# Kernel tuning notes

Hardware: AMD Instinct MI355X
Metric: run time of the kernel (lower is better)

Reference implementation:

```python
import jax, jax.numpy as jnp
import numpy as np

B, T, D_OBS = 64, 512, 128
D_LAT, D_HID, K = 16, 256, 8
VAR = 0.0005
LOG2PI = float(np.log(2.0 * np.pi))


def _leaky(x):
    return jnp.where(x > 0, x, 0.01 * x)


def setup_inputs() -> dict:
    key = jax.random.key(0)
    ks = jax.random.split(key, 12)
    s = 0.05
    return {
        "x": jax.random.normal(ks[0], (B, T, D_OBS), jnp.float32),
        "eps": jax.random.normal(ks[1], (B, T, D_LAT), jnp.float32),
        "W1": jax.random.normal(ks[2], (D_OBS, D_HID), jnp.float32) * s,
        "b1": jnp.zeros((D_HID,), jnp.float32),
        "W2": jax.random.normal(ks[3], (D_HID, 2 * D_LAT), jnp.float32) * s,
        "b2": jnp.zeros((2 * D_LAT,), jnp.float32),
        "Wt1": jax.random.normal(ks[4], (K, D_LAT, D_HID), jnp.float32) * s,
        "bt1": jnp.zeros((K, D_HID), jnp.float32),
        "Wt2": jax.random.normal(ks[5], (K, D_HID, D_LAT), jnp.float32) * s,
        "bt2": jnp.zeros((K, D_LAT), jnp.float32),
        "Wd1": jax.random.normal(ks[6], (D_LAT, D_HID), jnp.float32) * s,
        "bd1": jnp.zeros((D_HID,), jnp.float32),
        "Wd2": jax.random.normal(ks[7], (D_HID, D_OBS), jnp.float32) * s,
        "bd2": jnp.zeros((D_OBS,), jnp.float32),
        "Q": jax.random.normal(ks[8], (K, K), jnp.float32) * 0.1,
        "pi": jax.random.normal(ks[9], (K,), jnp.float32) * 0.1,
        "init_mean": jax.random.normal(ks[10], (K, D_LAT), jnp.float32),
        "init_cov": jax.random.uniform(ks[11], (K, 1, 1), jnp.float32) * jnp.eye(D_LAT, dtype=jnp.float32)[None] * 5.0,
        "covs": jnp.tile(jnp.eye(D_LAT, dtype=jnp.float32)[None], (K, 1, 1)),
    }


def _mvn_logprob(diff, chol):
    # diff [..., K, d]; chol [K, d, d] lower Cholesky of per-state covariance
    d = chol.shape[-1]
    Linv = jax.scipy.linalg.solve_triangular(
        chol, jnp.broadcast_to(jnp.eye(d, dtype=chol.dtype), chol.shape), lower=True)
    sol = jnp.einsum('kij,...kj->...ki', Linv, diff)
    logdet = 2.0 * jnp.sum(jnp.log(jnp.diagonal(chol, axis1=-2, axis2=-1)), -1)  # [K]
    return -0.5 * (d * LOG2PI + logdet + jnp.sum(sol * sol, -1))


def _forward(x, eps, W1, b1, W2, b2, Wt1, bt1, Wt2, bt2, Wd1, bd1, Wd2, bd2,
             Q, pi, init_mean, init_cov, covs):
    Bx = x.shape[0]
    dz = init_mean.shape[-1]
    # ---- factored MLP encoder: x -> (mu, logvar); reparameterized sample ----
    h = _leaky(x @ W1 + b1)
    enc = h @ W2 + b2
    z_mu, z_log_var = enc[..., :dz], enc[..., dz:]
    z = z_mu + jnp.exp(0.5 * z_log_var) * eps                            # [B,T,dz]
    # ---- local evidence log p(z_t | z_{t-1}, s_t=k) ----
    jitter = 1e-6 * jnp.eye(dz, dtype=x.dtype)
    L0 = jnp.linalg.cholesky(init_cov @ jnp.swapaxes(init_cov, -1, -2) + jitter)
    ev1 = _mvn_logprob(z[:, 0:1, None, :] - init_mean[None, None], L0)   # [B,1,K]
    ht = jax.nn.softplus(jnp.einsum('btd,kdh->btkh', z[:, :-1], Wt1) + bt1)
    means = jnp.einsum('btkh,khd->btkd', ht, Wt2) + bt2                  # [B,T-1,K,dz]
    Lt = jnp.linalg.cholesky(covs @ jnp.swapaxes(covs, -1, -2) + jitter)
    evT = _mvn_logprob(z[:, 1:, None, :] - means, Lt)                    # [B,T-1,K]
    ev = jnp.concatenate([ev1, evT], axis=1)                             # [B,T,K]
    # ---- HMM alpha recursion in log domain (temperature=1) ----
    log_pi = jax.nn.log_softmax(pi)
    Qlog = jax.nn.log_softmax(Q, axis=-1).T                              # [new, old]
    lp0 = ev[:, 0] + log_pi
    lZ0 = jax.scipy.special.logsumexp(lp0, axis=-1)
    la0 = lp0 - lZ0[:, None]

    def step(la, ev_t):
        lp = jax.scipy.special.logsumexp(ev_t[:, :, None] + Qlog[None] + la[:, None, :], axis=-1)
        lZ = jax.scipy.special.logsumexp(lp, axis=-1)
        return lp - lZ[:, None], lZ

    _, lZs = jax.lax.scan(step, la0, jnp.moveaxis(ev[:, 1:], 1, 0))
    log_Z = lZ0 + jnp.sum(lZs, axis=0)                                   # [B]
    # ---- decoder ----
    x_hat = _leaky(z @ Wd1 + bd1) @ Wd2 + bd2
    # ---- ELBO ----
    recon = jnp.sum(-0.5 * jnp.log(2.0 * jnp.pi * VAR) - (x - x_hat) ** 2 / (2.0 * VAR)) / Bx
    logq = -0.5 * (dz * LOG2PI + jnp.sum(z_log_var, -1)
                   + jnp.sum((z - z_mu) ** 2 / jnp.exp(z_log_var), -1))
    entropy_q = -jnp.sum(logq) / Bx
    msm = jnp.sum(log_Z) / Bx
    loss = -(recon + entropy_q + msm)
    return x_hat, z, loss


def reference(x, eps, W1, b1, W2, b2, Wt1, bt1, Wt2, bt2, Wd1, bd1, Wd2, bd2,
              Q, pi, init_mean, init_cov, covs):
    return _forward(x, eps, W1, b1, W2, b2, Wt1, bt1, Wt2, bt2, Wd1, bd1, Wd2, bd2,
                    Q, pi, init_mean, init_cov, covs)
```

## Files before the change

kernel.cpp:

```cpp
#include <hip/hip_runtime.h>
#include <math.h>

#define B_SZ   64
#define T_SZ   512
#define DOBS   128
#define DLAT   16
#define DHID   256
#define K_SZ   8
#define ROWS_A 32768

#define LOG2PI_F 1.8378770664093453f
#define VAR_F    5.0e-4f

#define LINV0_OFF   16
#define LOGDET0_OFF 2064
#define LINVT_OFF   2080
#define LOGDETT_OFF 4128
#define CVEC_OFF    4224
#define WIMG_F_OFF  8192

#define EVT_W1   0
#define EVT_W2   49152
#define EVT_LINV 82944
#define ENC_W1   86016
#define ENC_W2   120832
#define DEC_W1   129280
#define DEC_W2   135424
#define WCVT_TOTAL 182272

#define Z_OUT_OFF   4194304
#define LOSS_OFF    4718592
#define PBUF_OFF  262144

typedef __attribute__((ext_vector_type(8))) short short8;
typedef __attribute__((ext_vector_type(8))) unsigned short ush8;
typedef __attribute__((ext_vector_type(4))) float floatx4;

__device__ __forceinline__ float leakyf(float v) { return v > 0.f ? v : 0.01f * v; }
__device__ __forceinline__ unsigned short f2bf(float f) {
  union { float f; unsigned int u; } v; v.f = f;
  unsigned int lsb = (v.u >> 16) & 1;
  v.u += 0x7fffu + lsb;
  return (unsigned short)(v.u >> 16);
}
__device__ __forceinline__ unsigned int cvt_pk_bf16(float lo, float hi) {
  unsigned int r;
  asm("v_cvt_pk_bf16_f32 %0, %1, %2" : "=v"(r) : "v"(lo), "v"(hi));
  return r;
}
__device__ __forceinline__ float softplus_fast(float v) {
  return __logf(1.f + __expf(v));
}
__device__ __forceinline__ int permk(int kk) {
  return (kk & ~31) | ((kk & 15) << 1) | ((kk >> 4) & 1);
}

__global__ __launch_bounds__(256) void prep_kernel(const float* __restrict__ init_cov,
                                                   const float* __restrict__ covs,
                                                   const float* __restrict__ Wt2,
                                                   const float* __restrict__ bt2,
                                                   float* __restrict__ ws,
                                                   float* __restrict__ w2l) {
  __shared__ float M[16][16];
  __shared__ float L[16][16];
  __shared__ float X[16][17];
  int job = blockIdx.x;
  const float* C = (job < 8) ? (init_cov + job * 256) : (covs + (job - 8) * 256);
  float* linv = ws + ((job < 8) ? (LINV0_OFF + job * 256) : (LINVT_OFF + (job - 8) * 256));
  float* logdet = ws + ((job < 8) ? (LOGDET0_OFF + job) : (LOGDETT_OFF + (job - 8)));
  int tid = threadIdx.x;
  if (job == 0 && tid < 8) ws[tid] = 0.f;
  int i = tid >> 4, j = tid & 15;
  {
    float s = (i == j) ? 1e-6f : 0.f;
    #pragma unroll
    for (int p = 0; p < 16; ++p) s += C[i * 16 + p] * C[j * 16 + p];
    M[i][j] = s;
  }
  __syncthreads();
  for (int c = 0; c < 16; ++c) {
    if (tid == 0) {
      float s = M[c][c];
      for (int p = 0; p < c; ++p) s -= L[c][p] * L[c][p];
      L[c][c] = sqrtf(s);
    }
    __syncthreads();
    if (tid > c && tid < 16) {
      float s = M[tid][c];
      for (int p = 0; p < c; ++p) s -= L[tid][p] * L[c][p];
      L[tid][c] = s / L[c][c];
    }
    __syncthreads();
  }
  if (tid < 16) {
    for (int r = 0; r < 16; ++r) {
      float s = (r == tid) ? 1.f : 0.f;
      for (int p = tid; p < r; ++p) s -= L[r][p] * X[p][tid];
      X[r][tid] = (r >= tid) ? s / L[r][r] : 0.f;
    }
  }
  __syncthreads();
  linv[i * 16 + j] = X[i][j];
  if (tid == 0) {
    float s = 0.f;
    for (int d = 0; d < 16; ++d) s += logf(L[d][d]);
    *logdet = 2.f * s;
  }
  if (job >= 8) {
    int k = job - 8;
    const float* wrow = Wt2 + (long)k * 4096 + tid * 16;
    float* orow = w2l + (long)k * 4096 + tid * 16;
    #pragma unroll
    for (int i2 = 0; i2 < 16; ++i2) {
      float s = 0.f;
      for (int jj = 0; jj <= i2; ++jj) s += wrow[jj] * X[i2][jj];
      orow[i2] = s;
    }
    if (tid < 16) {
      float s = 0.f;
      const float* b = bt2 + k * 16;
      for (int jj = 0; jj <= tid; ++jj) s += b[jj] * X[tid][jj];
      ws[CVEC_OFF + k * 16 + tid] = s;
    }
  }
}

__global__ __launch_bounds__(256) void wcvt_kernel(
    const float* __restrict__ Wt1, const float* __restrict__ bt1,
    const float* __restrict__ W1, const float* __restrict__ W2,
    const float* __restrict__ Wd1, const float* __restrict__ bd1,
    const float* __restrict__ Wd2,
    const float* __restrict__ ws, const float* __restrict__ w2l,
    unsigned short* __restrict__ wimg) {
  for (int e = blockIdx.x * 256 + threadIdx.x; e < WCVT_TOTAL; e += gridDim.x * 256) {
    if (e < 65536) {
      int k = e >> 13, r = e & 8191, ch = r >> 5, d = r & 31;
      if (d < 24) {
        float v = (d < 16) ? Wt1[k * 4096 + d * 256 + ch]
                           : ((d == 16) ? bt1[k * 256 + ch] : 0.f);
        wimg[EVT_W1 + k * 6144 + ch * 24 + d] = f2bf(v);
      }
    } else if (e < 98304) {
      int e2 = e - 65536; int k = e2 >> 12, r = e2 & 4095, d2 = r >> 8, h = r & 255;
      wimg[EVT_W2 + k * 4224 + d2 * 264 + permk(h)] = f2bf(w2l[(long)k * 4096 + h * 16 + d2]);
    } else if (e < 100352) {
      int e2 = e - 98304; int k = e2 >> 8, r = e2 & 255, i = r >> 4, j = r & 15;
      wimg[EVT_LINV + k * 384 + i * 24 + j] = f2bf(ws[LINVT_OFF + k * 256 + i * 16 + j]);
    } else if (e < 133120) {
      int e2 = e - 100352; int n = e2 >> 7, kk = e2 & 127;
      wimg[ENC_W1 + n * 136 + kk] = f2bf(W1[kk * 256 + n]);
    } else if (e < 141312) {
      int e2 = e - 133120; int n = e2 >> 8, kk = e2 & 255;
      wimg[ENC_W2 + n * 264 + permk(kk)] = f2bf(W2[kk * 32 + n]);
    } else if (e < 149504) {
      int e2 = e - 141312; int n = e2 >> 5, d = e2 & 31;
      if (d < 24) {
        float v = (d < 16) ? Wd1[d * 256 + n] : ((d == 16) ? bd1[n] : 0.f);
        wimg[DEC_W1 + n * 24 + d] = f2bf(v);
      }
    } else {
      int e2 = e - 149504; int kk = e2 >> 7, n = e2 & 127;
      wimg[DEC_W2 + n * 264 + permk(kk)] = f2bf(Wd2[kk * 128 + n]);
    }
  }
}

__global__ __launch_bounds__(256) void enc_kernel(
    const float* __restrict__ x, const float* __restrict__ eps,
    const float* __restrict__ b1, const float* __restrict__ b2,
    const unsigned short* __restrict__ wimg,
    float* __restrict__ z_out, float* __restrict__ ws) {
  __shared__ __align__(16) unsigned short w2t[32 * 264];
  __shared__ __align__(16) unsigned short ttile[4][16 * 56];
  __shared__ float b1s[256];
  __shared__ float sred;
  int tid = threadIdx.x;
  if (tid == 0) sred = 0.f;
  {
    const ush8* s2 = (const ush8*)(wimg + ENC_W2);
    for (int e = tid; e < 1056; e += 256) ((ush8*)w2t)[e] = s2[e];
    b1s[tid] = b1[tid];
  }
  __syncthreads();

  int wid = tid >> 6, lane = tid & 63;
  int m = lane & 15, quad = lane >> 4;
  unsigned short* tt = ttile[wid];
  const unsigned short* w1i = wimg + ENC_W1;
  long rowb = (long)blockIdx.x * 64 + wid * 16;

  short8 xa[4];
  const float* xp = x + (rowb + m) * 128 + quad * 8;
  #pragma unroll
  for (int kt = 0; kt < 4; ++kt) {
    float4 f0 = *(const float4*)(xp + kt * 32);
    float4 f1 = *(const float4*)(xp + kt * 32 + 4);
    union { unsigned int u[4]; short8 s; } cv;
    cv.u[0] = cvt_pk_bf16(f0.x, f0.y);
    cv.u[1] = cvt_pk_bf16(f0.z, f0.w);
    cv.u[2] = cvt_pk_bf16(f1.x, f1.y);
    cv.u[3] = cvt_pk_bf16(f1.z, f1.w);
    xa[kt] = cv.s;
  }
  float bm0 = b2[m], bm1 = b2[16 + m];
  floatx4 a20 = {bm0, bm0, bm0, bm0};
  floatx4 a21 = {bm1, bm1, bm1, bm1};
  #pragma unroll
  for (int cp = 0; cp < 8; ++cp) {
    floatx4 a1h[2];
    #pragma unroll
    for (int h = 0; h < 2; ++h) {
      int c = cp * 2 + h;
      float bias = b1s[c * 16 + m];
      floatx4 a1 = {bias, bias, bias, bias};
      #pragma unroll
      for (int kt = 0; kt < 4; ++kt) {
        short8 bf = *(const short8*)&w1i[(c * 16 + m) * 136 + kt * 32 + quad * 8];
        a1 = __builtin_amdgcn_mfma_f32_16x16x32_bf16(xa[kt], bf, a1, 0, 0, 0);
      }
      a1h[h] = a1;
    }
    #pragma unroll
    for (int g = 0; g < 4; ++g) {
      unsigned int p = cvt_pk_bf16(leakyf(a1h[0][g]), leakyf(a1h[1][g]));
      *(unsigned int*)&tt[(quad * 4 + g) * 56 + 2 * m] = p;
    }
    short8 ha = *(const short8*)&tt[m * 56 + quad * 8];
    short8 wb0 = *(const short8*)&w2t[m * 264 + cp * 32 + quad * 8];
    short8 wb1 = *(const short8*)&w2t[(16 + m) * 264 + cp * 32 + quad * 8];
    a20 = __builtin_amdgcn_mfma_f32_16x16x32_bf16(ha, wb0, a20, 0, 0, 0);
    a21 = __builtin_amdgcn_mfma_f32_16x16x32_bf16(ha, wb1, a21, 0, 0, 0);
  }
  float logq_acc = 0.f;
  #pragma unroll
  for (int g = 0; g < 4; ++g) {
    long row = rowb + quad * 4 + g;
    float mu = a20[g], lv = a21[g];
    float ev = eps[row * 16 + m];
    float zv = mu + __expf(0.5f * lv) * ev;
    z_out[row * 16 + m] = zv;
    float zz = zv - mu;
    logq_acc += lv + zz * zz * __expf(-lv);
  }
  #pragma unroll
  for (int off = 1; off < 64; off <<= 1) logq_acc += __shfl_xor(logq_acc, off, 64);
  if (lane == 0) atomicAdd(&sred, -0.5f * logq_acc);
  __syncthreads();
  if (tid == 0) atomicAdd(&ws[1], sred - 0.5f * 16.f * LOG2PI_F * 64.f);
}

__global__ __launch_bounds__(256, 8) void evt_kernel(
    const float* __restrict__ z, const unsigned short* __restrict__ wimg,
    const float* __restrict__ ws, float* __restrict__ evT) {
  __shared__ __align__(16) unsigned short w2t[4224];
  __shared__ __align__(16) unsigned short ttile[4][16 * 56];
  __shared__ __align__(16) unsigned short linvb[384];
  int tid = threadIdx.x;
  int k = blockIdx.y;
  {
    const ush8* s2 = (const ush8*)(wimg + EVT_W2 + k * 4224);
    for (int e = tid; e < 528; e += 256) ((ush8*)w2t)[e] = s2[e];
    if (tid < 48) ((ush8*)linvb)[tid] = ((const ush8*)(wimg + EVT_LINV + k * 384))[tid];
  }
  float logdetk = ws[LOGDETT_OFF + k];
  __syncthreads();

  int wid = tid >> 6, lane = tid & 63;
  int m = lane & 15, quad = lane >> 4;
  unsigned short* tt = ttile[wid];
  const unsigned short* w1i = wimg + EVT_W1 + k * 6144;
  float cval = ws[CVEC_OFF + k * 16 + m];

  for (int tile = 0; tile < 2; ++tile) {
    long rowb = (long)blockIdx.x * 128 + wid * 32 + tile * 16;
    short8 za = (short8)0;
    if (quad < 2) {
      const float* zp = z + (rowb + m) * 16 + quad * 8;
      float4 f0 = *(const float4*)zp;
      float4 f1 = *(const float4*)(zp + 4);
      union { unsigned int u[4]; short8 s; } cv;
      cv.u[0] = cvt_pk_bf16(f0.x, f0.y);
      cv.u[1] = cvt_pk_bf16(f0.z, f0.w);
      cv.u[2] = cvt_pk_bf16(f1.x, f1.y);
      cv.u[3] = cvt_pk_bf16(f1.z, f1.w);
      za = cv.s;
    } else if (quad == 2) {
      za[0] = (short)0x3F80;
    }
    short8 za2 = (short8)0;
    if (quad < 2) {
      long r2 = rowb + m + 1; if (r2 > 32767) r2 = 32767;
      const float* zp2 = z + r2 * 16 + quad * 8;
      float4 f0 = *(const float4*)zp2;
      float4 f1 = *(const float4*)(zp2 + 4);
      union { unsigned int u[4]; short8 s; } cv;
      cv.u[0] = cvt_pk_bf16(f0.x, f0.y);
      cv.u[1] = cvt_pk_bf16(f0.z, f0.w);
      cv.u[2] = cvt_pk_bf16(f1.x, f1.y);
      cv.u[3] = cvt_pk_bf16(f1.z, f1.w);
      za2 = cv.s;
    }
    floatx4 a2 = {cval, cval, cval, cval};
    #pragma unroll
    for (int cp = 0; cp < 8; ++cp) {
      floatx4 a1h[2];
      #pragma unroll
      for (int h = 0; h < 2; ++h) {
        int c = cp * 2 + h;
        short8 bfrag = (short8)0;
        if (quad < 3) bfrag = *(const short8*)&w1i[(c * 16 + m) * 24 + quad * 8];
        floatx4 a1 = {0.f, 0.f, 0.f, 0.f};
        a1 = __builtin_amdgcn_mfma_f32_16x16x32_bf16(za, bfrag, a1, 0, 0, 0);
        a1h[h] = a1;
      }
      #pragma unroll
      for (int g = 0; g < 4; ++g) {
        unsigned int p = cvt_pk_bf16(softplus_fast(a1h[0][g]), softplus_fast(a1h[1][g]));
        *(unsigned int*)&tt[(quad * 4 + g) * 56 + 2 * m] = p;
      }
      short8 ha = *(const short8*)&tt[m * 56 + quad * 8];
      short8 wb = *(const short8*)&w2t[m * 264 + cp * 32 + quad * 8];
      a2 = __builtin_amdgcn_mfma_f32_16x16x32_bf16(ha, wb, a2, 0, 0, 0);
    }
    short8 lb = (short8)0;
    if (quad < 2) lb = *(const short8*)&linvb[m * 24 + quad * 8];
    floatx4 a3 = {0.f, 0.f, 0.f, 0.f};
    a3 = __builtin_amdgcn_mfma_f32_16x16x32_bf16(za2, lb, a3, 0, 0, 0);
    #pragma unroll
    for (int g = 0; g < 4; ++g) {
      float v = a3[g] - a2[g];
      v = v * v;
      v += __shfl_xor(v, 1, 64);
      v += __shfl_xor(v, 2, 64);
      v += __shfl_xor(v, 4, 64);
      v += __shfl_xor(v, 8, 64);
      long grow = rowb + quad * 4 + g;
      if (m == 0 && (grow & 511) != 511) {
        long r1 = grow + 1;
        evT[(r1 >> 9) * 4096 + (long)k * 512 + (r1 & 511)] =
            -0.5f * (16.f * LOG2PI_F + logdetk + v);
      }
    }
  }
}

__global__ __launch_bounds__(1024) void hmm_fused(
    const float* __restrict__ Q, const float* __restrict__ pi,
    const float* __restrict__ z, const float* __restrict__ init_mean,
    const float* __restrict__ evT, float* __restrict__ ws) {
  __shared__ float sP[16][64];
  __shared__ float sacc[16];
  int tid = threadIdx.x;
  int c = tid >> 6, lane = tid & 63;
  int b = blockIdx.x;
  int i = lane >> 3, j = lane & 7;

  float qp[8];
  #pragma unroll
  for (int p = 0; p < 8; ++p) {
    float mr = Q[p * 8 + 0];
    #pragma unroll
    for (int cc = 1; cc < 8; ++cc) mr = fmaxf(mr, Q[p * 8 + cc]);
    float rs = 0.f;
    #pragma unroll
    for (int cc = 0; cc < 8; ++cc) rs += __expf(Q[p * 8 + cc] - mr);
    qp[p] = __expf(Q[p * 8 + i] - mr) / rs;
  }
  float qself;
  {
    float mr = Q[j * 8 + 0];
    #pragma unroll
    for (int cc = 1; cc < 8; ++cc) mr = fmaxf(mr, Q[j * 8 + cc]);
    float rs = 0.f;
    #pragma unroll
    for (int cc = 0; cc < 8; ++cc) rs += __expf(Q[j * 8 + cc] - mr);
    qself = __expf(Q[j * 8 + i] - mr) / rs;
  }

  int t0 = 1 + c * 32;
  int L = (c == 15) ? 31 : 32;
  const float* evI = evT + (long)b * 4096 + (long)i * 512 + t0;

  float f[32];
  float accm = 0.f;
  #pragma unroll
  for (int s = 0; s < 32; ++s) {
    float e = (s < L) ? evI[s] : 0.f;
    float m = e;
    m = fmaxf(m, __shfl_xor(m, 8, 64));
    m = fmaxf(m, __shfl_xor(m, 16, 64));
    m = fmaxf(m, __shfl_xor(m, 32, 64));
    f[s] = __expf(e - m);
    if (s < L) accm += m;
  }

  float P = f[0] * qself;
  #pragma unroll
  for (int s = 1; s < 32; ++s) {
    if (s < L) {
      float a0 = __shfl(P, j,      64);
      float a1 = __shfl(P, 8 + j,  64);
      float a2 = __shfl(P, 16 + j, 64);
      float a3 = __shfl(P, 24 + j, 64);
      float a4 = __shfl(P, 32 + j, 64);
      float a5 = __shfl(P, 40 + j, 64);
      float a6 = __shfl(P, 48 + j, 64);
      float a7 = __shfl(P, 56 + j, 64);
      float sv = ((qp[0] * a0 + qp[1] * a1) + (qp[2] * a2 + qp[3] * a3))
               + ((qp[4] * a4 + qp[5] * a5) + (qp[6] * a6 + qp[7] * a7));
      P = f[s] * sv;
    }
    if ((s & 7) == 7) {
      float mx = P;
      mx = fmaxf(mx, __shfl_xor(mx, 1, 64));
      mx = fmaxf(mx, __shfl_xor(mx, 2, 64));
      mx = fmaxf(mx, __shfl_xor(mx, 4, 64));
      mx = fmaxf(mx, __shfl_xor(mx, 8, 64));
      mx = fmaxf(mx, __shfl_xor(mx, 16, 64));
      mx = fmaxf(mx, __shfl_xor(mx, 32, 64));
      mx = fmaxf(mx, 1e-30f);
      P = P / mx;
      accm += __logf(mx);
    }
  }
  sP[c][lane] = P;
  if (lane == 0) sacc[c] = accm;
  __syncthreads();

  if (c == 0) {
    float mp = pi[0];
    #pragma unroll
    for (int cc = 1; cc < 8; ++cc) mp = fmaxf(mp, pi[cc]);
    float sp = 0.f;
    #pragma unroll
    for (int cc = 0; cc < 8; ++cc) sp += __expf(pi[cc] - mp);
    float lpi = pi[j] - mp - __logf(sp);

    const float* zr = z + (long)b * 8192;
    const float* linv = ws + LINV0_OFF + j * 256;
    float diff[16];
    #pragma unroll
    for (int d = 0; d < 16; ++d) diff[d] = zr[d] - init_mean[j * 16 + d];
    float quad0 = 0.f;
    #pragma unroll
    for (int i2 = 0; i2 < 16; ++i2) {
      float s = 0.f;
      #pragma unroll
      for (int jj = 0; jj < 16; ++jj) s += linv[i2 * 16 + jj] * diff[jj];
      quad0 += s * s;
    }
    float ev0 = -0.5f * (16.f * LOG2PI_F + ws[LOGDET0_OFF + j] + quad0);

    float lp0 = ev0 + lpi;
    float m0 = lp0;
    m0 = fmaxf(m0, __shfl_xor(m0, 1, 64));
    m0 = fmaxf(m0, __shfl_xor(m0, 2, 64));
    m0 = fmaxf(m0, __shfl_xor(m0, 4, 64));
    float u = __expf(lp0 - m0);
    double acc = (double)m0;

    #pragma unroll
    for (int cc2 = 0; cc2 < 16; ++cc2) {
      float Pc = sP[cc2][lane];
      float contrib = Pc * u;
      contrib += __shfl_xor(contrib, 1, 64);
      contrib += __shfl_xor(contrib, 2, 64);
      contrib += __shfl_xor(contrib, 4, 64);
      u = __shfl(contrib, j * 9, 64);
      float mxu = u;
      mxu = fmaxf(mxu, __shfl_xor(mxu, 1, 64));
      mxu = fmaxf(mxu, __shfl_xor(mxu, 2, 64));
      mxu = fmaxf(mxu, __shfl_xor(mxu, 4, 64));
      mxu = fmaxf(mxu, 1e-30f);
      u = u / mxu;
      acc += (double)(__logf(mxu) + sacc[cc2]);
    }
    float su = u;
    su += __shfl_xor(su, 1, 64);
    su += __shfl_xor(su, 2, 64);
    su += __shfl_xor(su, 4, 64);
    float logZ = (float)(acc + (double)__logf(su));
    if (lane == 0) atomicAdd(&ws[2], logZ);
  }
}

__global__ __launch_bounds__(256) void dec_kernel(
    const float* __restrict__ x, const float* __restrict__ z,
    const float* __restrict__ bd2,
    const unsigned short* __restrict__ wimg,
    float* __restrict__ xhat, float* __restrict__ ws) {
  __shared__ __align__(16) unsigned short w1t[6144];
  __shared__ __align__(16) unsigned short ttile[4][16 * 56];
  __shared__ float bd2s[128];
  __shared__ float sred;
  int tid = threadIdx.x;
  if (tid == 0) sred = 0.f;
  {
    const ush8* s1 = (const ush8*)(wimg + DEC_W1);
    for (int e = tid; e < 768; e += 256) ((ush8*)w1t)[e] = s1[e];
    if (tid < 128) bd2s[tid] = bd2[tid];
  }
  __syncthreads();

  int wid = tid >> 6, lane = tid & 63;
  int m = lane & 15, quad = lane >> 4;
  unsigned short* tt = ttile[wid];
  const unsigned short* w2i = wimg + DEC_W2;
  long rowb = (long)blockIdx.x * 64 + wid * 16;

  short8 za = (short8)0;
  if (quad < 2) {
    const float* zp = z + (rowb + m) * 16 + quad * 8;
    float4 f0 = *(const float4*)zp;
    float4 f1 = *(const float4*)(zp + 4);
    union { unsigned int u[4]; short8 s; } cv;
    cv.u[0] = cvt_pk_bf16(f0.x, f0.y);
    cv.u[1] = cvt_pk_bf16(f0.z, f0.w);
    cv.u[2] = cvt_pk_bf16(f1.x, f1.y);
    cv.u[3] = cvt_pk_bf16(f1.z, f1.w);
    za = cv.s;
  } else if (quad == 2) {
    za[0] = (short)0x3F80;
  }
  floatx4 a2[8];
  #pragma unroll
  for (int c2 = 0; c2 < 8; ++c2) {
    float bv = bd2s[c2 * 16 + m];
    a2[c2] = (floatx4){bv, bv, bv, bv};
  }
  #pragma unroll
  for (int cp = 0; cp < 8; ++cp) {
    floatx4 a1h[2];
    #pragma unroll
    for (int h = 0; h < 2; ++h) {
      int c = cp * 2 + h;
      short8 bfrag = (short8)0;
      if (quad < 3) bfrag = *(const short8*)&w1t[(c * 16 + m) * 24 + quad * 8];
      floatx4 a1 = {0.f, 0.f, 0.f, 0.f};
      a1 = __builtin_amdgcn_mfma_f32_16x16x32_bf16(za, bfrag, a1, 0, 0, 0);
      a1h[h] = a1;
    }
    #pragma unroll
    for (int g = 0; g < 4; ++g) {
      unsigned int p = cvt_pk_bf16(leakyf(a1h[0][g]), leakyf(a1h[1][g]));
      *(unsigned int*)&tt[(quad * 4 + g) * 56 + 2 * m] = p;
    }
    short8 ha = *(const short8*)&tt[m * 56 + quad * 8];
    #pragma unroll
    for (int c2 = 0; c2 < 8; ++c2) {
      short8 wb = *(const short8*)&w2i[(c2 * 16 + m) * 264 + cp * 32 + quad * 8];
      a2[c2] = __builtin_amdgcn_mfma_f32_16x16x32_bf16(ha, wb, a2[c2], 0, 0, 0);
    }
  }
  const float C0 = -0.5f * logf(6.2831853071795864f * VAR_F);
  float rsum = 0.f;
  #pragma unroll
  for (int c2 = 0; c2 < 8; ++c2) {
    int col = c2 * 16 + m;
    #pragma unroll
    for (int g = 0; g < 4; ++g) {
      long row = rowb + quad * 4 + g;
      float xh = a2[c2][g];
      xhat[row * 128 + col] = xh;
      float dd = x[row * 128 + col] - xh;
      rsum += C0 - dd * dd * (0.5f / VAR_F);
    }
  }
  #pragma unroll
  for (int off = 1; off < 64; off <<= 1) rsum += __shfl_xor(rsum, off, 64);
  if (lane == 0) atomicAdd(&sred, rsum);
  __syncthreads();
  if (tid == 0) {
    atomicAdd(&ws[0], sred);
    __threadfence();
    unsigned int t = atomicAdd((unsigned int*)(ws + 4), 1u);
    if (t == gridDim.x - 1) {
      __threadfence();
      float recon = atomicAdd(&ws[0], 0.f);
      float loss = -((recon - ws[1] + ws[2]) * (1.f / 64.f));
      xhat[LOSS_OFF] = loss;
    }
  }
}

extern "C" void kernel_launch(void* const* d_in, const int* in_sizes, int n_in,
                              void* d_out, int out_size, void* d_ws, size_t ws_size,
                              hipStream_t stream) {
  (void)in_sizes; (void)n_in; (void)out_size; (void)ws_size;
  const float* x   = (const float*)d_in[0];
  const float* eps = (const float*)d_in[1];
  const float* W1  = (const float*)d_in[2];
  const float* b1  = (const float*)d_in[3];
  const float* W2  = (const float*)d_in[4];
  const float* b2  = (const float*)d_in[5];
  const float* Wt1 = (const float*)d_in[6];
  const float* bt1 = (const float*)d_in[7];
  const float* Wt2 = (const float*)d_in[8];
  const float* bt2 = (const float*)d_in[9];
  const float* Wd1 = (const float*)d_in[10];
  const float* bd1 = (const float*)d_in[11];
  const float* Wd2 = (const float*)d_in[12];
  const float* bd2 = (const float*)d_in[13];
  const float* Q   = (const float*)d_in[14];
  const float* pi  = (const float*)d_in[15];
  const float* im  = (const float*)d_in[16];
  const float* ic  = (const float*)d_in[17];
  const float* cv  = (const float*)d_in[18];
  float* out = (float*)d_out;
  float* ws  = (float*)d_ws;
  float* z_out = out + Z_OUT_OFF;
  float* evT  = out;
  float* w2l  = out + PBUF_OFF;
  unsigned short* wimg = (unsigned short*)(ws + WIMG_F_OFF);

  prep_kernel<<<16, 256, 0, stream>>>(ic, cv, Wt2, bt2, ws, w2l);
  wcvt_kernel<<<144, 256, 0, stream>>>(Wt1, bt1, W1, W2, Wd1, bd1, Wd2, ws, w2l, wimg);
  enc_kernel<<<512, 256, 0, stream>>>(x, eps, b1, b2, wimg, z_out, ws);
  evt_kernel<<<dim3(256, 8), 256, 0, stream>>>(z_out, wimg, ws, evT);
  hmm_fused<<<64, 1024, 0, stream>>>(Q, pi, z_out, im, evT, ws);
  dec_kernel<<<512, 256, 0, stream>>>(x, z_out, bd2, wimg, out, ws);
}
```

Before: 245.2 us.

## Fuse decoder into evidence kernel and finalize loss in HMM kernel

Merges the decoder blocks into the evidence-computation launch as extra grid columns, so decoder work runs alongside the evidence blocks instead of after the HMM recursion. Because the decoder now writes x_hat before the HMM runs, the evidence buffer moves from the output to workspace, and the HMM kernel performs the last-block loss finalization. This removes one launch and lets the decoder overlap the evidence work, at the cost of lower occupancy from the combined register footprint (launch bounds 6 instead of 8). The serial HMM kernel remains the tail.

```diff
diff --git a/kernel.cpp b/kernel.cpp
--- a/kernel.cpp
+++ b/kernel.cpp
@@ -18,6 +18,7 @@
 #define LOGDETT_OFF 4128
 #define CVEC_OFF    4224
 #define WIMG_F_OFF  8192
+#define EVT_WS_OFF  131072
 
 #define EVT_W1   0
 #define EVT_W2   49152
@@ -249,30 +250,118 @@
   if (tid == 0) atomicAdd(&ws[1], sred - 0.5f * 16.f * LOG2PI_F * 64.f);
 }
 
-__global__ __launch_bounds__(256, 8) void evt_kernel(
-    const float* __restrict__ z, const unsigned short* __restrict__ wimg,
-    const float* __restrict__ ws, float* __restrict__ evT) {
-  __shared__ __align__(16) unsigned short w2t[4224];
+__global__ __launch_bounds__(256, 6) void evtdec_kernel(
+    const float* __restrict__ x, const float* __restrict__ z,
+    const float* __restrict__ bd2,
+    const unsigned short* __restrict__ wimg,
+    float* __restrict__ evT, float* __restrict__ xhat,
+    float* __restrict__ ws) {
+  __shared__ __align__(16) unsigned short wbuf[6144];
   __shared__ __align__(16) unsigned short ttile[4][16 * 56];
-  __shared__ __align__(16) unsigned short linvb[384];
+  __shared__ float fbuf[132];
   int tid = threadIdx.x;
-  int k = blockIdx.y;
-  {
-    const ush8* s2 = (const ush8*)(wimg + EVT_W2 + k * 4224);
-    for (int e = tid; e < 528; e += 256) ((ush8*)w2t)[e] = s2[e];
-    if (tid < 48) ((ush8*)linvb)[tid] = ((const ush8*)(wimg + EVT_LINV + k * 384))[tid];
-  }
-  float logdetk = ws[LOGDETT_OFF + k];
-  __syncthreads();
-
   int wid = tid >> 6, lane = tid & 63;
   int m = lane & 15, quad = lane >> 4;
   unsigned short* tt = ttile[wid];
-  const unsigned short* w1i = wimg + EVT_W1 + k * 6144;
-  float cval = ws[CVEC_OFF + k * 16 + m];
-
-  for (int tile = 0; tile < 2; ++tile) {
-    long rowb = (long)blockIdx.x * 128 + wid * 32 + tile * 16;
+
+  if (blockIdx.x < 256) {
+    int k = blockIdx.y;
+    {
+      const ush8* s2 = (const ush8*)(wimg + EVT_W2 + k * 4224);
+      for (int e = tid; e < 528; e += 256) ((ush8*)wbuf)[e] = s2[e];
+      if (tid < 48) ((ush8*)(wbuf + 4224))[tid] = ((const ush8*)(wimg + EVT_LINV + k * 384))[tid];
+    }
+    float logdetk = ws[LOGDETT_OFF + k];
+    __syncthreads();
+    const unsigned short* w2t = wbuf;
+    const unsigned short* linvb = wbuf + 4224;
+    const unsigned short* w1i = wimg + EVT_W1 + k * 6144;
+    float cval = ws[CVEC_OFF + k * 16 + m];
+
+    for (int tile = 0; tile < 2; ++tile) {
+      long rowb = (long)blockIdx.x * 128 + wid * 32 + tile * 16;
+      short8 za = (short8)0;
+      if (quad < 2) {
+        const float* zp = z + (rowb + m) * 16 + quad * 8;
+        float4 f0 = *(const float4*)zp;
+        float4 f1 = *(const float4*)(zp + 4);
+        union { unsigned int u[4]; short8 s; } cv;
+        cv.u[0] = cvt_pk_bf16(f0.x, f0.y);
+        cv.u[1] = cvt_pk_bf16(f0.z, f0.w);
+        cv.u[2] = cvt_pk_bf16(f1.x, f1.y);
+        cv.u[3] = cvt_pk_bf16(f1.z, f1.w);
+        za = cv.s;
+      } else if (quad == 2) {
+        za[0] = (short)0x3F80;
+      }
+      short8 za2 = (short8)0;
+      if (quad < 2) {
+        long r2 = rowb + m + 1; if (r2 > 32767) r2 = 32767;
+        const float* zp2 = z + r2 * 16 + quad * 8;
+        float4 f0 = *(const float4*)zp2;
+        float4 f1 = *(const float4*)(zp2 + 4);
+        union { unsigned int u[4]; short8 s; } cv;
+        cv.u[0] = cvt_pk_bf16(f0.x, f0.y);
+        cv.u[1] = cvt_pk_bf16(f0.z, f0.w);
+        cv.u[2] = cvt_pk_bf16(f1.x, f1.y);
+        cv.u[3] = cvt_pk_bf16(f1.z, f1.w);
+        za2 = cv.s;
+      }
+      floatx4 a2 = {cval, cval, cval, cval};
+      #pragma unroll
+      for (int cp = 0; cp < 8; ++cp) {
+        floatx4 a1h[2];
+        #pragma unroll
+        for (int h = 0; h < 2; ++h) {
+          int c = cp * 2 + h;
+          short8 bfrag = (short8)0;
+          if (quad < 3) bfrag = *(const short8*)&w1i[(c * 16 + m) * 24 + quad * 8];
+          floatx4 a1 = {0.f, 0.f, 0.f, 0.f};
+          a1 = __builtin_amdgcn_mfma_f32_16x16x32_bf16(za, bfrag, a1, 0, 0, 0);
+          a1h[h] = a1;
+        }
+        #pragma unroll
+        for (int g = 0; g < 4; ++g) {
+          unsigned int p = cvt_pk_bf16(softplus_fast(a1h[0][g]), softplus_fast(a1h[1][g]));
+          *(unsigned int*)&tt[(quad * 4 + g) * 56 + 2 * m] = p;
+        }
+        short8 ha = *(const short8*)&tt[m * 56 + quad * 8];
+        short8 wb = *(const short8*)&w2t[m * 264 + cp * 32 + quad * 8];
+        a2 = __builtin_amdgcn_mfma_f32_16x16x32_bf16(ha, wb, a2, 0, 0, 0);
+      }
+      short8 lb = (short8)0;
+      if (quad < 2) lb = *(const short8*)&linvb[m * 24 + quad * 8];
+      floatx4 a3 = {0.f, 0.f, 0.f, 0.f};
+      a3 = __builtin_amdgcn_mfma_f32_16x16x32_bf16(za2, lb, a3, 0, 0, 0);
+      #pragma unroll
+      for (int g = 0; g < 4; ++g) {
+        float v = a3[g] - a2[g];
+        v = v * v;
+        v += __shfl_xor(v, 1, 64);
+        v += __shfl_xor(v, 2, 64);
+        v += __shfl_xor(v, 4, 64);
+        v += __shfl_xor(v, 8, 64);
+        long grow = rowb + quad * 4 + g;
+        if (m == 0 && (grow & 511) != 511) {
+          long r1 = grow + 1;
+          evT[(r1 >> 9) * 4096 + (long)k * 512 + (r1 & 511)] =
+              -0.5f * (16.f * LOG2PI_F + logdetk + v);
+        }
+      }
+    }
+  } else {
+    int decb = blockIdx.y * 64 + ((int)blockIdx.x - 256);
+    if (tid == 0) fbuf[128] = 0.f;
+    {
+      const ush8* s1 = (const ush8*)(wimg + DEC_W1);
+      for (int e = tid; e < 768; e += 256) ((ush8*)wbuf)[e] = s1[e];
+      if (tid < 128) fbuf[tid] = bd2[tid];
+    }
+    __syncthreads();
+    const unsigned short* w1t = wbuf;
+    const unsigned short* w2i = wimg + DEC_W2;
+    long rowb = (long)decb * 64 + wid * 16;
+
     short8 za = (short8)0;
     if (quad < 2) {
       const float* zp = z + (rowb + m) * 16 + quad * 8;
@@ -287,20 +376,12 @@
     } else if (quad == 2) {
       za[0] = (short)0x3F80;
     }
-    short8 za2 = (short8)0;
-    if (quad < 2) {
-      long r2 = rowb + m + 1; if (r2 > 32767) r2 = 32767;
-      const float* zp2 = z + r2 * 16 + quad * 8;
-      float4 f0 = *(const float4*)zp2;
-      float4 f1 = *(const float4*)(zp2 + 4);
-      union { unsigned int u[4]; short8 s; } cv;
-      cv.u[0] = cvt_pk_bf16(f0.x, f0.y);
-      cv.u[1] = cvt_pk_bf16(f0.z, f0.w);
-      cv.u[2] = cvt_pk_bf16(f1.x, f1.y);
-      cv.u[3] = cvt_pk_bf16(f1.z, f1.w);
-      za2 = cv.s;
-    }
-    floatx4 a2 = {cval, cval, cval, cval};
+    floatx4 a2[8];
+    #pragma unroll
+    for (int c2 = 0; c2 < 8; ++c2) {
+      float bv = fbuf[c2 * 16 + m];
+      a2[c2] = (floatx4){bv, bv, bv, bv};
+    }
     #pragma unroll
     for (int cp = 0; cp < 8; ++cp) {
       floatx4 a1h[2];
@@ -308,46 +389,50 @@
       for (int h = 0; h < 2; ++h) {
         int c = cp * 2 + h;
         short8 bfrag = (short8)0;
-        if (quad < 3) bfrag = *(const short8*)&w1i[(c * 16 + m) * 24 + quad * 8];
+        if (quad < 3) bfrag = *(const short8*)&w1t[(c * 16 + m) * 24 + quad * 8];
         floatx4 a1 = {0.f, 0.f, 0.f, 0.f};
         a1 = __builtin_amdgcn_mfma_f32_16x16x32_bf16(za, bfrag, a1, 0, 0, 0);
         a1h[h] = a1;
       }
       #pragma unroll
       for (int g = 0; g < 4; ++g) {
-        unsigned int p = cvt_pk_bf16(softplus_fast(a1h[0][g]), softplus_fast(a1h[1][g]));
+        unsigned int p = cvt_pk_bf16(leakyf(a1h[0][g]), leakyf(a1h[1][g]));
         *(unsigned int*)&tt[(quad * 4 + g) * 56 + 2 * m] = p;
       }
       short8 ha = *(const short8*)&tt[m * 56 + quad * 8];
-      short8 wb = *(const short8*)&w2t[m * 264 + cp * 32 + quad * 8];
-      a2 = __builtin_amdgcn_mfma_f32_16x16x32_bf16(ha, wb, a2, 0, 0, 0);
-    }
-    short8 lb = (short8)0;
-    if (quad < 2) lb = *(const short8*)&linvb[m * 24 + quad * 8];
-    floatx4 a3 = {0.f, 0.f, 0.f, 0.f};
-    a3 = __builtin_amdgcn_mfma_f32_16x16x32_bf16(za2, lb, a3, 0, 0, 0);
-    #pragma unroll
-    for (int g = 0; g < 4; ++g) {
-      float v = a3[g] - a2[g];
-      v = v * v;
-      v += __shfl_xor(v, 1, 64);
-      v += __shfl_xor(v, 2, 64);
-      v += __shfl_xor(v, 4, 64);
-      v += __shfl_xor(v, 8, 64);
-      long grow = rowb + quad * 4 + g;
-      if (m == 0 && (grow & 511) != 511) {
-        long r1 = grow + 1;
-        evT[(r1 >> 9) * 4096 + (long)k * 512 + (r1 & 511)] =
-            -0.5f * (16.f * LOG2PI_F + logdetk + v);
-      }
-    }
+      #pragma unroll
+      for (int c2 = 0; c2 < 8; ++c2) {
+        short8 wb = *(const short8*)&w2i[(c2 * 16 + m) * 264 + cp * 32 + quad * 8];
+        a2[c2] = __builtin_amdgcn_mfma_f32_16x16x32_bf16(ha, wb, a2[c2], 0, 0, 0);
+      }
+    }
+    const float C0 = -0.5f * logf(6.2831853071795864f * VAR_F);
+    float rsum = 0.f;
+    #pragma unroll
+    for (int c2 = 0; c2 < 8; ++c2) {
+      int col = c2 * 16 + m;
+      #pragma unroll
+      for (int g = 0; g < 4; ++g) {
+        long row = rowb + quad * 4 + g;
+        float xh = a2[c2][g];
+        xhat[row * 128 + col] = xh;
+        float dd = x[row * 128 + col] - xh;
+        rsum += C0 - dd * dd * (0.5f / VAR_F);
+      }
+    }
+    #pragma unroll
+    for (int off = 1; off < 64; off <<= 1) rsum += __shfl_xor(rsum, off, 64);
+    if (lane == 0) atomicAdd(&fbuf[128], rsum);
+    __syncthreads();
+    if (tid == 0) atomicAdd(&ws[0], fbuf[128]);
   }
 }
 
 __global__ __launch_bounds__(1024) void hmm_fused(
     const float* __restrict__ Q, const float* __restrict__ pi,
     const float* __restrict__ z, const float* __restrict__ init_mean,
-    const float* __restrict__ evT, float* __restrict__ ws) {
+    const float* __restrict__ evT, float* __restrict__ xhat,
+    float* __restrict__ ws) {
   __shared__ float sP[16][64];
   __shared__ float sacc[16];
   int tid = threadIdx.x;
@@ -480,105 +565,16 @@
     su += __shfl_xor(su, 2, 64);
     su += __shfl_xor(su, 4, 64);
     float logZ = (float)(acc + (double)__logf(su));
-    if (lane == 0) atomicAdd(&ws[2], logZ);
-  }
-}
-
-__global__ __launch_bounds__(256) void dec_kernel(
-    const float* __restrict__ x, const float* __restrict__ z,
-    const float* __restrict__ bd2,
-    const unsigned short* __restrict__ wimg,
-    float* __restrict__ xhat, float* __restrict__ ws) {
-  __shared__ __align__(16) unsigned short w1t[6144];
-  __shared__ __align__(16) unsigned short ttile[4][16 * 56];
-  __shared__ float bd2s[128];
-  __shared__ float sred;
-  int tid = threadIdx.x;
-  if (tid == 0) sred = 0.f;
-  {
-    const ush8* s1 = (const ush8*)(wimg + DEC_W1);
-    for (int e = tid; e < 768; e += 256) ((ush8*)w1t)[e] = s1[e];
-    if (tid < 128) bd2s[tid] = bd2[tid];
-  }
-  __syncthreads();
-
-  int wid = tid >> 6, lane = tid & 63;
-  int m = lane & 15, quad = lane >> 4;
-  unsigned short* tt = ttile[wid];
-  const unsigned short* w2i = wimg + DEC_W2;
-  long rowb = (long)blockIdx.x * 64 + wid * 16;
-
-  short8 za = (short8)0;
-  if (quad < 2) {
-    const float* zp = z + (rowb + m) * 16 + quad * 8;
-    float4 f0 = *(const float4*)zp;
-    float4 f1 = *(const float4*)(zp + 4);
-    union { unsigned int u[4]; short8 s; } cv;
-    cv.u[0] = cvt_pk_bf16(f0.x, f0.y);
-    cv.u[1] = cvt_pk_bf16(f0.z, f0.w);
-    cv.u[2] = cvt_pk_bf16(f1.x, f1.y);
-    cv.u[3] = cvt_pk_bf16(f1.z, f1.w);
-    za = cv.s;
-  } else if (quad == 2) {
-    za[0] = (short)0x3F80;
-  }
-  floatx4 a2[8];
-  #pragma unroll
-  for (int c2 = 0; c2 < 8; ++c2) {
-    float bv = bd2s[c2 * 16 + m];
-    a2[c2] = (floatx4){bv, bv, bv, bv};
-  }
-  #pragma unroll
-  for (int cp = 0; cp < 8; ++cp) {
-    floatx4 a1h[2];
-    #pragma unroll
-    for (int h = 0; h < 2; ++h) {
-      int c = cp * 2 + h;
-      short8 bfrag = (short8)0;
-      if (quad < 3) bfrag = *(const short8*)&w1t[(c * 16 + m) * 24 + quad * 8];
-      floatx4 a1 = {0.f, 0.f, 0.f, 0.f};
-      a1 = __builtin_amdgcn_mfma_f32_16x16x32_bf16(za, bfrag, a1, 0, 0, 0);
-      a1h[h] = a1;
-    }
-    #pragma unroll
-    for (int g = 0; g < 4; ++g) {
-      unsigned int p = cvt_pk_bf16(leakyf(a1h[0][g]), leakyf(a1h[1][g]));
-      *(unsigned int*)&tt[(quad * 4 + g) * 56 + 2 * m] = p;
-    }
-    short8 ha = *(const short8*)&tt[m * 56 + quad * 8];
-    #pragma unroll
-    for (int c2 = 0; c2 < 8; ++c2) {
-      short8 wb = *(const short8*)&w2i[(c2 * 16 + m) * 264 + cp * 32 + quad * 8];
-      a2[c2] = __builtin_amdgcn_mfma_f32_16x16x32_bf16(ha, wb, a2[c2], 0, 0, 0);
-    }
-  }
-  const float C0 = -0.5f * logf(6.2831853071795864f * VAR_F);
-  float rsum = 0.f;
-  #pragma unroll
-  for (int c2 = 0; c2 < 8; ++c2) {
-    int col = c2 * 16 + m;
-    #pragma unroll
-    for (int g = 0; g < 4; ++g) {
-      long row = rowb + quad * 4 + g;
-      float xh = a2[c2][g];
-      xhat[row * 128 + col] = xh;
-      float dd = x[row * 128 + col] - xh;
-      rsum += C0 - dd * dd * (0.5f / VAR_F);
-    }
-  }
-  #pragma unroll
-  for (int off = 1; off < 64; off <<= 1) rsum += __shfl_xor(rsum, off, 64);
-  if (lane == 0) atomicAdd(&sred, rsum);
-  __syncthreads();
-  if (tid == 0) {
-    atomicAdd(&ws[0], sred);
-    __threadfence();
-    unsigned int t = atomicAdd((unsigned int*)(ws + 4), 1u);
-    if (t == gridDim.x - 1) {
+    if (lane == 0) {
+      atomicAdd(&ws[2], logZ);
       __threadfence();
-      float recon = atomicAdd(&ws[0], 0.f);
-      float loss = -((recon - ws[1] + ws[2]) * (1.f / 64.f));
-      xhat[LOSS_OFF] = loss;
+      unsigned int t = atomicAdd((unsigned int*)(ws + 5), 1u);
+      if (t == gridDim.x - 1) {
+        __threadfence();
+        float msm = atomicAdd(&ws[2], 0.f);
+        float loss = -((ws[0] - ws[1] + msm) * (1.f / 64.f));
+        xhat[LOSS_OFF] = loss;
+      }
     }
   }
 }
@@ -609,14 +605,13 @@
   float* out = (float*)d_out;
   float* ws  = (float*)d_ws;
   float* z_out = out + Z_OUT_OFF;
-  float* evT  = out;
+  float* evT  = ws + EVT_WS_OFF;
   float* w2l  = out + PBUF_OFF;
   unsigned short* wimg = (unsigned short*)(ws + WIMG_F_OFF);
 
   prep_kernel<<<16, 256, 0, stream>>>(ic, cv, Wt2, bt2, ws, w2l);
   wcvt_kernel<<<144, 256, 0, stream>>>(Wt1, bt1, W1, W2, Wd1, bd1, Wd2, ws, w2l, wimg);
   enc_kernel<<<512, 256, 0, stream>>>(x, eps, b1, b2, wimg, z_out, ws);
-  evt_kernel<<<dim3(256, 8), 256, 0, stream>>>(z_out, wimg, ws, evT);
-  hmm_fused<<<64, 1024, 0, stream>>>(Q, pi, z_out, im, evT, ws);
-  dec_kernel<<<512, 256, 0, stream>>>(x, z_out, bd2, wimg, out, ws);
-}
+  evtdec_kernel<<<dim3(320, 8), 256, 0, stream>>>(x, z_out, bd2, wimg, evT, out, ws);
+  hmm_fused<<<64, 1024, 0, stream>>>(Q, pi, z_out, im, evT, out, ws);
+}
```

New measurement: 218.0 us. 1.12x faster.
